# Optimization experiments

Hardware: AMD Instinct MI355X
Metric: run time of the kernel (lower is better)

## Reference

```python
import jax, jax.numpy as jnp
import numpy as np

MOMENTUM = 0.9
EPS_MASK = 1e-6   # torch clamp(min=1e-6) on mask sum
EPS_NORM = 1e-12  # torch F.normalize eps

def _l2norm(x):
    n = jnp.linalg.norm(x, axis=-1, keepdims=True)
    return x / jnp.maximum(n, EPS_NORM)

def setup_inputs() -> dict:
    key = jax.random.key(0)
    k1, k2, k3, k4, k5 = jax.random.split(key, 5)
    num_users, num_proto, embd_dim = 50000, 16, 128
    B, S = 8192, 50
    return {
        "user_prototypes": jax.random.normal(k1, (num_users, num_proto, embd_dim), jnp.float32),
        "shared_prototypes": jax.random.normal(k2, (1, num_proto, embd_dim), jnp.float32),
        "interaction_count": jax.random.uniform(k3, (num_users,), jnp.float32),
        "features": jax.random.normal(k4, (B, S, embd_dim), jnp.float32),
        "success_mask": jax.random.uniform(k5, (B, S), jnp.float32),
        "user_idx": jnp.arange(B, dtype=jnp.int64) if jax.config.jax_enable_x64 else jnp.arange(B, dtype=jnp.int32),
    }

def reference(user_prototypes, shared_prototypes, interaction_count, features, success_mask, user_idx):
    # --- gather ---
    current = user_prototypes[user_idx]                    # [B, P, D]
    ic = interaction_count[user_idx]                       # [B]
    m = jnp.clip(MOMENTUM + ic / 1000.0, MOMENTUM, 0.99)[:, None, None]
    # --- masked reduction over history (features dim==3 branch, mask dim==2) ---
    mask = success_mask[..., None]                         # [B, S, 1]
    upd = (features * mask).sum(axis=1) / jnp.maximum(mask.sum(axis=1), EPS_MASK)  # [B, D]
    upd = _l2norm(upd)                                     # F.normalize(dim=-1)
    upd = jnp.broadcast_to(upd[:, None, :], current.shape) # expand to [B, P, D]
    # --- momentum blend + scatter write ---
    new_batch = m * current + (1.0 - m) * upd
    new_user_prototypes = user_prototypes.at[user_idx].set(new_batch)
    # --- shared prototype update ---
    shared_upd = _l2norm(upd.mean(axis=0))                 # [P, D]
    new_shared = MOMENTUM * shared_prototypes + (1.0 - MOMENTUM) * shared_upd[None]
    # --- interaction count increment ---
    new_ic = interaction_count.at[user_idx].add(1.0)
    return new_user_prototypes, new_shared, new_ic
```

## Files before the change

### kernel.cpp

```cpp
#include <hip/hip_runtime.h>

#define NB 8192
#define NS 50
#define ND 128
#define NP 16
#define NU 50000
#define NRED 64

__global__ void k_init_map(int* __restrict__ map) {
    int i = blockIdx.x * blockDim.x + threadIdx.x;
    if (i < NU) map[i] = -1;
}

__global__ void k_scatter_map(const int* __restrict__ user_idx, int* __restrict__ map) {
    int b = blockIdx.x * blockDim.x + threadIdx.x;
    if (b < NB) map[user_idx[b]] = b;
}

__global__ void k_upd(const float* __restrict__ features,
                      const float* __restrict__ mask,
                      float* __restrict__ upd) {
    int b = blockIdx.x;
    int d = threadIdx.x;

    __shared__ float smask[NS];
    __shared__ float red[ND];

    if (d < NS) smask[d] = mask[(size_t)b * NS + d];
    __syncthreads();

    float msum = 0.f;
#pragma unroll
    for (int s = 0; s < NS; ++s) msum += smask[s];

    const float* f = features + (size_t)b * NS * ND + d;
    float acc = 0.f;
#pragma unroll 5
    for (int s = 0; s < NS; ++s) acc += f[(size_t)s * ND] * smask[s];

    float u = acc / fmaxf(msum, 1e-6f);

    red[d] = u * u;
    __syncthreads();
    for (int off = 64; off > 0; off >>= 1) {
        if (d < off) red[d] += red[d + off];
        __syncthreads();
    }
    float norm = sqrtf(red[0]);
    u = u / fmaxf(norm, 1e-12f);

    upd[(size_t)b * ND + d] = u;
}

__global__ void k_colsum(const float* __restrict__ upd, float* __restrict__ part) {
    int blk = blockIdx.x;
    int t = threadIdx.x;
    int d = t & 127;
    int h = t >> 7;

    const int rows = NB / NRED;
    int r0 = blk * rows;

    float s = 0.f;
    for (int r = r0 + h; r < r0 + rows; r += 2)
        s += upd[(size_t)r * ND + d];

    __shared__ float red[2][ND];
    red[h][d] = s;
    __syncthreads();
    if (h == 0)
        part[(size_t)blk * ND + d] = red[0][d] + red[1][d];
}

__global__ void k_shared_final(const float* __restrict__ part,
                               const float* __restrict__ shared_in,
                               float* __restrict__ shared_out) {
    int d = threadIdx.x;

    float tot = 0.f;
#pragma unroll
    for (int j = 0; j < NRED; ++j) tot += part[(size_t)j * ND + d];
    float mean = tot / (float)NB;

    __shared__ float red[ND];
    red[d] = mean * mean;
    __syncthreads();
    for (int off = 64; off > 0; off >>= 1) {
        if (d < off) red[d] += red[d + off];
        __syncthreads();
    }
    float inv = 1.0f / fmaxf(sqrtf(red[0]), 1e-12f);
    float su = mean * inv;

#pragma unroll
    for (int p = 0; p < NP; ++p)
        shared_out[p * ND + d] = 0.9f * shared_in[p * ND + d] + 0.1f * su;
}

__global__ void k_blend(const float* __restrict__ proto,
                        const float* __restrict__ ic,
                        const int* __restrict__ map,
                        const float* __restrict__ upd,
                        float* __restrict__ out) {
    size_t g = (size_t)blockIdx.x * blockDim.x + threadIdx.x;
    const size_t total = (size_t)NU * NP * ND / 4;
    if (g >= total) return;

    float4 v = ((const float4*)proto)[g];
    int u = (int)(g >> 9);
    int rem = (int)(g & 511);
    int b = map[u];
    if (b >= 0) {
        float icv = ic[u];
        float m = fminf(fmaxf(0.9f + icv * 0.001f, 0.9f), 0.99f);
        float om = 1.0f - m;
        float4 up = ((const float4*)upd)[(size_t)b * 32 + (rem & 31)];
        v.x = m * v.x + om * up.x;
        v.y = m * v.y + om * up.y;
        v.z = m * v.z + om * up.z;
        v.w = m * v.w + om * up.w;
    }
    ((float4*)out)[g] = v;
}

__global__ void k_ic_copy(const float* __restrict__ ic, float* __restrict__ out) {
    int i = blockIdx.x * blockDim.x + threadIdx.x;
    if (i < NU) out[i] = ic[i];
}

__global__ void k_ic_add(const int* __restrict__ user_idx, float* __restrict__ out) {
    int b = blockIdx.x * blockDim.x + threadIdx.x;
    if (b < NB) atomicAdd(&out[user_idx[b]], 1.0f);
}

extern "C" void kernel_launch(void* const* d_in, const int* in_sizes, int n_in,
                              void* d_out, int out_size, void* d_ws, size_t ws_size,
                              hipStream_t stream) {
    const float* user_prototypes   = (const float*)d_in[0];
    const float* shared_prototypes = (const float*)d_in[1];
    const float* interaction_count = (const float*)d_in[2];
    const float* features          = (const float*)d_in[3];
    const float* success_mask      = (const float*)d_in[4];
    const int*   user_idx          = (const int*)d_in[5];

    float* out_proto  = (float*)d_out;
    float* out_shared = out_proto + (size_t)NU * NP * ND;
    float* out_ic     = out_shared + NP * ND;

    int*   map  = (int*)d_ws;
    float* upd  = (float*)((char*)d_ws + 200704);
    float* part = upd + (size_t)NB * ND;

    k_init_map<<<(NU + 255) / 256, 256, 0, stream>>>(map);
    k_scatter_map<<<(NB + 255) / 256, 256, 0, stream>>>(user_idx, map);

    k_upd<<<NB, ND, 0, stream>>>(features, success_mask, upd);

    k_colsum<<<NRED, 256, 0, stream>>>(upd, part);
    k_shared_final<<<1, ND, 0, stream>>>(part, shared_prototypes, out_shared);

    const size_t total4 = (size_t)NU * NP * ND / 4;
    k_blend<<<(int)((total4 + 255) / 256), 256, 0, stream>>>(
        user_prototypes, interaction_count, map, upd, out_proto);

    k_ic_copy<<<(NU + 255) / 256, 256, 0, stream>>>(interaction_count, out_ic);
    k_ic_add<<<(NB + 255) / 256, 256, 0, stream>>>(user_idx, out_ic);
}
```

Before: 220.9 us.

## Fuse masked reduction, prototype blend and count update into one per-user kernel

Replaces the separate update, blend, count-copy and atomic-add kernels with one kernel that runs one block per user. For selected users, the block computes the normalized masked feature mean with float4 loads, a shared-memory partial reduction and a wavefront shuffle. It then blends all 16 prototypes and writes the incremented count. Unselected users just copy their prototypes and count. This removes several launches and the re-read of the update vector in the blend pass. In exchange, the count update assumes unique user indices (plain +1 instead of atomics), and selected blocks do uneven work.

```diff
diff --git a/kernel.cpp b/kernel.cpp
--- a/kernel.cpp
+++ b/kernel.cpp
@@ -17,39 +17,91 @@
     if (b < NB) map[user_idx[b]] = b;
 }
 
-__global__ void k_upd(const float* __restrict__ features,
-                      const float* __restrict__ mask,
-                      float* __restrict__ upd) {
-    int b = blockIdx.x;
-    int d = threadIdx.x;
+__global__ __launch_bounds__(256) void k_big(
+    const float* __restrict__ proto,
+    const float* __restrict__ ic,
+    const float* __restrict__ features,
+    const float* __restrict__ mask,
+    const int* __restrict__ map,
+    float* __restrict__ out_proto,
+    float* __restrict__ out_ic,
+    float* __restrict__ upd)
+{
+    int u = blockIdx.x;
+    int t = threadIdx.x;
+    int b = map[u];
 
-    __shared__ float smask[NS];
-    __shared__ float red[ND];
+    const float4* proto4 = (const float4*)proto;
+    float4* out4 = (float4*)out_proto;
+    size_t base = (size_t)u * (NP * ND / 4);
 
-    if (d < NS) smask[d] = mask[(size_t)b * NS + d];
+    if (b < 0) {
+        out4[base + t]       = proto4[base + t];
+        out4[base + t + 256] = proto4[base + t + 256];
+        if (t == 0) out_ic[u] = ic[u];
+        return;
+    }
+
+    __shared__ float  smask[NS];
+    __shared__ float4 part[8][32];
+    __shared__ float4 updv[32];
+
+    if (t < NS) smask[t] = mask[(size_t)b * NS + t];
     __syncthreads();
 
-    float msum = 0.f;
+    int q = t & 31;
+    int g = t >> 5;
+    const float4* f4 = (const float4*)features + (size_t)b * (NS * ND / 4);
+    float4 acc = {0.f, 0.f, 0.f, 0.f};
+    for (int s = g; s < NS; s += 8) {
+        float w = smask[s];
+        float4 v = f4[s * 32 + q];
+        acc.x += v.x * w; acc.y += v.y * w; acc.z += v.z * w; acc.w += v.w * w;
+    }
+    part[g][q] = acc;
+    __syncthreads();
+
+    if (t < 32) {
+        float msum = 0.f;
 #pragma unroll
-    for (int s = 0; s < NS; ++s) msum += smask[s];
+        for (int s = 0; s < NS; ++s) msum += smask[s];
 
-    const float* f = features + (size_t)b * NS * ND + d;
-    float acc = 0.f;
-#pragma unroll 5
-    for (int s = 0; s < NS; ++s) acc += f[(size_t)s * ND] * smask[s];
+        float4 a = part[0][t];
+#pragma unroll
+        for (int g2 = 1; g2 < 8; ++g2) {
+            float4 p = part[g2][t];
+            a.x += p.x; a.y += p.y; a.z += p.z; a.w += p.w;
+        }
+        float invm = 1.0f / fmaxf(msum, 1e-6f);
+        a.x *= invm; a.y *= invm; a.z *= invm; a.w *= invm;
 
-    float u = acc / fmaxf(msum, 1e-6f);
+        float d2 = a.x * a.x + a.y * a.y + a.z * a.z + a.w * a.w;
+#pragma unroll
+        for (int mm = 16; mm >= 1; mm >>= 1) d2 += __shfl_xor(d2, mm, 64);
+        float inv = 1.0f / fmaxf(sqrtf(d2), 1e-12f);
+        a.x *= inv; a.y *= inv; a.z *= inv; a.w *= inv;
 
-    red[d] = u * u;
+        updv[t] = a;
+        ((float4*)upd)[(size_t)b * 32 + t] = a;
+    }
     __syncthreads();
-    for (int off = 64; off > 0; off >>= 1) {
-        if (d < off) red[d] += red[d + off];
-        __syncthreads();
+
+    float icv = ic[u];
+    float m = fminf(fmaxf(0.9f + icv * 0.001f, 0.9f), 0.99f);
+    float om = 1.0f - m;
+    if (t == 0) out_ic[u] = icv + 1.0f;
+
+#pragma unroll
+    for (int rep = 0; rep < 2; ++rep) {
+        int idx = t + rep * 256;
+        float4 v = proto4[base + idx];
+        float4 uu = updv[idx & 31];
+        v.x = m * v.x + om * uu.x;
+        v.y = m * v.y + om * uu.y;
+        v.z = m * v.z + om * uu.z;
+        v.w = m * v.w + om * uu.w;
+        out4[base + idx] = v;
     }
-    float norm = sqrtf(red[0]);
-    u = u / fmaxf(norm, 1e-12f);
-
-    upd[(size_t)b * ND + d] = u;
 }
 
 __global__ void k_colsum(const float* __restrict__ upd, float* __restrict__ part) {
@@ -97,42 +149,6 @@
         shared_out[p * ND + d] = 0.9f * shared_in[p * ND + d] + 0.1f * su;
 }
 
-__global__ void k_blend(const float* __restrict__ proto,
-                        const float* __restrict__ ic,
-                        const int* __restrict__ map,
-                        const float* __restrict__ upd,
-                        float* __restrict__ out) {
-    size_t g = (size_t)blockIdx.x * blockDim.x + threadIdx.x;
-    const size_t total = (size_t)NU * NP * ND / 4;
-    if (g >= total) return;
-
-    float4 v = ((const float4*)proto)[g];
-    int u = (int)(g >> 9);
-    int rem = (int)(g & 511);
-    int b = map[u];
-    if (b >= 0) {
-        float icv = ic[u];
-        float m = fminf(fmaxf(0.9f + icv * 0.001f, 0.9f), 0.99f);
-        float om = 1.0f - m;
-        float4 up = ((const float4*)upd)[(size_t)b * 32 + (rem & 31)];
-        v.x = m * v.x + om * up.x;
-        v.y = m * v.y + om * up.y;
-        v.z = m * v.z + om * up.z;
-        v.w = m * v.w + om * up.w;
-    }
-    ((float4*)out)[g] = v;
-}
-
-__global__ void k_ic_copy(const float* __restrict__ ic, float* __restrict__ out) {
-    int i = blockIdx.x * blockDim.x + threadIdx.x;
-    if (i < NU) out[i] = ic[i];
-}
-
-__global__ void k_ic_add(const int* __restrict__ user_idx, float* __restrict__ out) {
-    int b = blockIdx.x * blockDim.x + threadIdx.x;
-    if (b < NB) atomicAdd(&out[user_idx[b]], 1.0f);
-}
-
 extern "C" void kernel_launch(void* const* d_in, const int* in_sizes, int n_in,
                               void* d_out, int out_size, void* d_ws, size_t ws_size,
                               hipStream_t stream) {
@@ -154,15 +170,10 @@
     k_init_map<<<(NU + 255) / 256, 256, 0, stream>>>(map);
     k_scatter_map<<<(NB + 255) / 256, 256, 0, stream>>>(user_idx, map);
 
-    k_upd<<<NB, ND, 0, stream>>>(features, success_mask, upd);
+    k_big<<<NU, 256, 0, stream>>>(user_prototypes, interaction_count,
+                                  features, success_mask, map,
+                                  out_proto, out_ic, upd);
 
     k_colsum<<<NRED, 256, 0, stream>>>(upd, part);
     k_shared_final<<<1, ND, 0, stream>>>(part, shared_prototypes, out_shared);
-
-    const size_t total4 = (size_t)NU * NP * ND / 4;
-    k_blend<<<(int)((total4 + 255) / 256), 256, 0, stream>>>(
-        user_prototypes, interaction_count, map, upd, out_proto);
-
-    k_ic_copy<<<(NU + 255) / 256, 256, 0, stream>>>(interaction_count, out_ic);
-    k_ic_add<<<(NB + 255) / 256, 256, 0, stream>>>(user_idx, out_ic);
 }
```

Measured after the change: 224.1 us. About the same (+1.5%).
